# Kernel optimization log

Measured on AMD Instinct MI355X. Metric: run time of the kernel, lower is better.

Reference implementation:

```python
import jax, jax.numpy as jnp
import numpy as np

# BEV grid config from __init__ defaults
X0, XS, BX = -50.0, 0.5, 200
Y0, YS, BY = -50.0, 0.5, 200
Z0, Z1, BZ = -10.0, 10.0, 20


def setup_inputs() -> dict:
    key = jax.random.key(0)
    k1, k2, k3 = jax.random.split(key, 3)
    B, N, D, H, W, C = 2, 6, 41, 28, 50, 64
    # ego-frame 3D points; range slightly larger than BEV bounds so some are invalid
    geometry = jax.random.uniform(k1, (B, N, D, H, W, 3), minval=-60.0, maxval=60.0)
    features = jax.random.normal(k2, (B, N, C, H, W), dtype=jnp.float32)
    # depth distribution over D bins per pixel
    depth_probs = jax.nn.softmax(jax.random.normal(k3, (B, N, D, H, W)), axis=2)
    return {"geometry": geometry, "features": features, "depth_probs": depth_probs}


def _pool_one(geom, feat, depth):
    # geom: [N, D, H, W, 3], feat: [N, C, H, W], depth: [N, D, H, W]
    x, y, z = geom[..., 0], geom[..., 1], geom[..., 2]
    # torch .long() truncates toward zero -> jnp.trunc
    xi = jnp.trunc((x - X0) / XS).astype(jnp.int32)
    yi = jnp.trunc((y - Y0) / YS).astype(jnp.int32)
    zi = jnp.trunc((z - Z0) / (Z1 - Z0) * BZ).astype(jnp.int32)
    valid = (xi >= 0) & (xi < BX) & (yi >= 0) & (yi < BY) & (zi >= 0) & (zi < BZ)
    lin = jnp.where(valid, (zi * BY + yi) * BX + xi, 0).reshape(-1)   # [P]
    w = jnp.where(valid, depth, 0.0).reshape(-1)                      # [P]
    N, C, H, W = feat.shape
    D = depth.shape[1]
    # expand per-pixel features across depth bins: [N, D, H, W, C] -> [P, C]
    feat_pts = jnp.broadcast_to(
        feat.transpose(0, 2, 3, 1)[:, None], (N, D, H, W, C)
    ).reshape(-1, C)
    vals = feat_pts * w[:, None]                                      # [P, C]
    voxel = jnp.zeros((BZ * BY * BX, C), dtype=vals.dtype).at[lin].add(vals)
    voxel = voxel.reshape(BZ, BY, BX, C)
    bev = voxel.max(axis=0)                                           # [BY, BX, C]
    return bev.transpose(2, 0, 1)                                     # [C, BY, BX]


def reference(geometry, features, depth_probs):
    # -> (B, C, bev_y, bev_x)
    return jax.vmap(_pool_one)(geometry, features, depth_probs)
```

## Files before the change

### kernel.cpp

```cpp
#include <hip/hip_runtime.h>
#include <hip/hip_bf16.h>

#define CC 64
#define HW 1400
#define DHW 57400
#define NPTS 688800
#define NCOL 80000
#define KCAP 24

#define OFF_CNT    0
#define OFF_BUCKET 320000
#define OFF_FEATT  15680000

static __device__ __forceinline__ unsigned short f32_to_bf16_rne(float v) {
    unsigned int u = __float_as_uint(v);
    unsigned int r = u + 0x7fffu + ((u >> 16) & 1u);
    return (unsigned short)(r >> 16);
}
static __device__ __forceinline__ float bf16_to_f32(unsigned short h) {
    return __uint_as_float((unsigned)h << 16);
}

__global__ __launch_bounds__(256) void kz_zero(int* __restrict__ cnt) {
    int i = blockIdx.x * 256 + threadIdx.x;
    if (i < NCOL) cnt[i] = 0;
}

__global__ __launch_bounds__(256) void k01_prep(const float* __restrict__ feat,
                                                const float* __restrict__ geom,
                                                const float* __restrict__ depth,
                                                unsigned short* __restrict__ feat_t,
                                                int* __restrict__ cnt,
                                                int2* __restrict__ bucket) {
    int bid = blockIdx.x;
    if (bid < 264) {
        __shared__ float tile[64][65];
        int bn  = bid / 22;
        int hw0 = (bid % 22) * 64;
        int wv   = threadIdx.x >> 6;
        int lane = threadIdx.x & 63;
        const float* src = feat + bn * CC * HW;
        #pragma unroll
        for (int i = 0; i < 16; ++i) {
            int c = wv * 16 + i, hw = hw0 + lane;
            if (hw < HW) tile[c][lane] = src[c * HW + hw];
        }
        __syncthreads();
        unsigned short* dst = feat_t + bn * HW * CC;
        #pragma unroll
        for (int i = 0; i < 16; ++i) {
            int hwl = wv * 16 + i, hw = hw0 + hwl;
            if (hw < HW) dst[hw * CC + lane] = f32_to_bf16_rne(tile[lane][hwl]);
        }
        return;
    }

    int pt = (bid - 264) * 256 + threadIdx.x;
    if (pt >= NPTS) return;

    float x = geom[3 * pt + 0];
    float y = geom[3 * pt + 1];
    float z = geom[3 * pt + 2];
    float w = depth[pt];

    float fx = (x + 50.0f) / 0.5f;
    float fy = (y + 50.0f) / 0.5f;
    float fz = (z + 10.0f) / 20.0f * 20.0f;
    int xi = (int)fx, yi = (int)fy, zi = (int)fz;

    bool valid = (xi >= 0) & (xi < 200) & (yi >= 0) & (yi < 200) & (zi >= 0) & (zi < 20);
    if (!valid) return;

    int bn  = pt / DHW;
    int hw  = (pt - bn * DHW) % HW;
    int b   = bn / 6;
    int col = b * 40000 + yi * 200 + xi;
    int pix = bn * HW + hw;

    int idx = atomicAdd(&cnt[col], 1);
    if (idx < KCAP)
        bucket[(size_t)col * KCAP + idx] =
            make_int2(__float_as_int(w), (pix << 5) | zi);
}

__global__ __launch_bounds__(1024) void k2_pool(const int* __restrict__ cnt,
                                                const int2* __restrict__ bucket,
                                                const unsigned short* __restrict__ feat_t,
                                                float* __restrict__ out) {
    __shared__ int2  lrec[64 * KCAP];
    __shared__ int   lcnt[64];
    __shared__ float buf[64][65];
    int tid  = threadIdx.x;
    int wv   = tid >> 6;
    int lane = tid & 63;
    int b    = blockIdx.x / 625;
    int yx0  = (blockIdx.x % 625) * 64;
    int colBase = b * 40000 + yx0;

    const int2* gsrc = bucket + (size_t)colBase * KCAP;
    lrec[tid] = gsrc[tid];
    if (tid < 64 * KCAP - 1024) lrec[1024 + tid] = gsrc[1024 + tid];
    if (tid < 64) lcnt[tid] = cnt[colBase + tid];
    __syncthreads();

    int   kk[4];
    int2  r0[4];
    float f0[4];
    #pragma unroll
    for (int j = 0; j < 4; ++j) {
        int col = wv * 4 + j;
        int kj = lcnt[col];
        kj = kj > KCAP ? KCAP : kj;
        kk[j] = __builtin_amdgcn_readfirstlane(kj);
        r0[j] = lrec[col * KCAP];
        unsigned pix = kk[j] > 0 ? (((unsigned)r0[j].y) >> 5) : 0u;
        pix = __builtin_amdgcn_readfirstlane(pix);
        f0[j] = bf16_to_f32(feat_t[pix * CC + lane]);
    }

    #pragma unroll
    for (int j = 0; j < 4; ++j) {
        int col = wv * 4 + j;
        int k = kk[j];
        const int2* rec = &lrec[col * KCAP];
        float m = 0.0f;

        if (k == 1) {
            m = fmaxf(0.0f, __int_as_float(r0[j].x) * f0[j]);
        } else if (k == 2) {
            int2 r1 = rec[1];
            unsigned px1 = __builtin_amdgcn_readfirstlane(((unsigned)r1.y) >> 5);
            float f1 = bf16_to_f32(feat_t[px1 * CC + lane]);
            float p0 = __int_as_float(r0[j].x) * f0[j];
            float p1 = __int_as_float(r1.x) * f1;
            int z0 = __builtin_amdgcn_readfirstlane(r0[j].y & 31);
            int z1 = __builtin_amdgcn_readfirstlane(r1.y & 31);
            m = (z0 == z1) ? fmaxf(0.0f, p0 + p1)
                           : fmaxf(0.0f, fmaxf(p0, p1));
        } else if (k == 3) {
            int2 r1 = rec[1], r2 = rec[2];
            unsigned px1 = __builtin_amdgcn_readfirstlane(((unsigned)r1.y) >> 5);
            unsigned px2 = __builtin_amdgcn_readfirstlane(((unsigned)r2.y) >> 5);
            float f1 = bf16_to_f32(feat_t[px1 * CC + lane]);
            float f2 = bf16_to_f32(feat_t[px2 * CC + lane]);
            float p0 = __int_as_float(r0[j].x) * f0[j];
            float p1 = __int_as_float(r1.x) * f1;
            float p2 = __int_as_float(r2.x) * f2;
            int z0 = __builtin_amdgcn_readfirstlane(r0[j].y & 31);
            int z1 = __builtin_amdgcn_readfirstlane(r1.y & 31);
            int z2 = __builtin_amdgcn_readfirstlane(r2.y & 31);
            bool e01 = (z0 == z1), e02 = (z0 == z2), e12 = (z1 == z2);
            if (e01 && e12)      m = fmaxf(0.0f, p0 + p1 + p2);
            else if (e01)        m = fmaxf(fmaxf(0.0f, p0 + p1), p2);
            else if (e02)        m = fmaxf(fmaxf(0.0f, p0 + p2), p1);
            else if (e12)        m = fmaxf(fmaxf(0.0f, p0), p1 + p2);
            else                 m = fmaxf(fmaxf(0.0f, p0), fmaxf(p1, p2));
        } else if (k >= 4) {
            unsigned handled = 0;
            for (int i = 0; i < k; ++i) {
                if ((handled >> i) & 1) continue;
                int2 ri = rec[i];
                int zi = __builtin_amdgcn_readfirstlane(ri.y & 31);
                unsigned pxi = __builtin_amdgcn_readfirstlane(((unsigned)ri.y) >> 5);
                float s = __int_as_float(ri.x) * bf16_to_f32(feat_t[pxi * CC + lane]);
                for (int t = i + 1; t < k; ++t) {
                    int2 rt = rec[t];
                    if (!((handled >> t) & 1) &&
                        __builtin_amdgcn_readfirstlane(rt.y & 31) == zi) {
                        unsigned pxt = __builtin_amdgcn_readfirstlane(((unsigned)rt.y) >> 5);
                        s += __int_as_float(rt.x) * bf16_to_f32(feat_t[pxt * CC + lane]);
                        handled |= 1u << t;
                    }
                }
                m = fmaxf(m, s);
            }
        }
        buf[col][lane] = m;
    }
    __syncthreads();
    #pragma unroll
    for (int i = 0; i < 4; ++i) {
        int c = wv * 4 + i;
        out[((size_t)b * CC + c) * 40000 + yx0 + lane] = buf[lane][c];
    }
}

extern "C" void kernel_launch(void* const* d_in, const int* in_sizes, int n_in,
                              void* d_out, int out_size, void* d_ws, size_t ws_size,
                              hipStream_t stream) {
    const float* geom  = (const float*)d_in[0];
    const float* feat  = (const float*)d_in[1];
    const float* depth = (const float*)d_in[2];
    float* out = (float*)d_out;

    char* ws = (char*)d_ws;
    int*            cnt    = (int*)(ws + OFF_CNT);
    int2*           bucket = (int2*)(ws + OFF_BUCKET);
    unsigned short* feat_t = (unsigned short*)(ws + OFF_FEATT);

    hipLaunchKernelGGL(kz_zero,  dim3(313),  dim3(256),  0, stream, cnt);
    hipLaunchKernelGGL(k01_prep, dim3(2955), dim3(256),  0, stream, feat, geom, depth, feat_t, cnt, bucket);
    hipLaunchKernelGGL(k2_pool,  dim3(1250), dim3(1024), 0, stream, cnt, bucket, feat_t, out);
}
```

Before: 35.72 us.

## Split buckets into hot/overflow arrays and read records directly in pool kernel

Bucket records are split into a compact first-8 array and an overflow array. The pool kernel now reads counts and the first two records straight from global memory with one 16-byte load, instead of staging the full 24-slot bucket block in LDS. The aim is to cut the mostly wasted traffic of copying all 24 slots per column when typical counts are small. Blocks shrink to 512 threads covering 32 columns, the zeroing kernel writes int4, and the output store is remapped. The cost is extra scattered global loads for columns holding 3 or more points.

Result: slower. 37.96 us (+6.3%).

```diff
diff --git a/kernel.cpp b/kernel.cpp
--- a/kernel.cpp
+++ b/kernel.cpp
@@ -7,9 +7,11 @@
 #define NPTS 688800
 #define NCOL 80000
 #define KCAP 24
+#define KA   8
 
 #define OFF_CNT    0
-#define OFF_BUCKET 320000
+#define OFF_BUCKA  320000
+#define OFF_BUCKB  5440000
 #define OFF_FEATT  15680000
 
 static __device__ __forceinline__ unsigned short f32_to_bf16_rne(float v) {
@@ -21,9 +23,9 @@
     return __uint_as_float((unsigned)h << 16);
 }
 
-__global__ __launch_bounds__(256) void kz_zero(int* __restrict__ cnt) {
+__global__ __launch_bounds__(256) void kz_zero(int4* __restrict__ cnt4) {
     int i = blockIdx.x * 256 + threadIdx.x;
-    if (i < NCOL) cnt[i] = 0;
+    if (i < NCOL / 4) cnt4[i] = make_int4(0, 0, 0, 0);
 }
 
 __global__ __launch_bounds__(256) void k01_prep(const float* __restrict__ feat,
@@ -31,7 +33,8 @@
                                                 const float* __restrict__ depth,
                                                 unsigned short* __restrict__ feat_t,
                                                 int* __restrict__ cnt,
-                                                int2* __restrict__ bucket) {
+                                                int2* __restrict__ bucketA,
+                                                int2* __restrict__ bucketB) {
     int bid = blockIdx.x;
     if (bid < 264) {
         __shared__ float tile[64][65];
@@ -78,76 +81,69 @@
     int pix = bn * HW + hw;
 
     int idx = atomicAdd(&cnt[col], 1);
-    if (idx < KCAP)
-        bucket[(size_t)col * KCAP + idx] =
-            make_int2(__float_as_int(w), (pix << 5) | zi);
-}
-
-__global__ __launch_bounds__(1024) void k2_pool(const int* __restrict__ cnt,
-                                                const int2* __restrict__ bucket,
-                                                const unsigned short* __restrict__ feat_t,
-                                                float* __restrict__ out) {
-    __shared__ int2  lrec[64 * KCAP];
-    __shared__ int   lcnt[64];
-    __shared__ float buf[64][65];
+    int2 rec = make_int2(__float_as_int(w), (pix << 5) | zi);
+    if (idx < KA)
+        bucketA[(size_t)col * KA + idx] = rec;
+    else if (idx < KCAP)
+        bucketB[(size_t)col * (KCAP - KA) + (idx - KA)] = rec;
+}
+
+__global__ __launch_bounds__(512) void k2_pool(const int* __restrict__ cnt,
+                                               const int2* __restrict__ bucketA,
+                                               const int2* __restrict__ bucketB,
+                                               const unsigned short* __restrict__ feat_t,
+                                               float* __restrict__ out) {
+    __shared__ float buf[32][65];
     int tid  = threadIdx.x;
     int wv   = tid >> 6;
     int lane = tid & 63;
-    int b    = blockIdx.x / 625;
-    int yx0  = (blockIdx.x % 625) * 64;
+    int b    = blockIdx.x / 1250;
+    int yx0  = (blockIdx.x % 1250) * 32;
     int colBase = b * 40000 + yx0;
 
-    const int2* gsrc = bucket + (size_t)colBase * KCAP;
-    lrec[tid] = gsrc[tid];
-    if (tid < 64 * KCAP - 1024) lrec[1024 + tid] = gsrc[1024 + tid];
-    if (tid < 64) lcnt[tid] = cnt[colBase + tid];
-    __syncthreads();
-
     int   kk[4];
-    int2  r0[4];
+    int4  r01[4];
     float f0[4];
     #pragma unroll
     for (int j = 0; j < 4; ++j) {
-        int col = wv * 4 + j;
-        int kj = lcnt[col];
+        int col = colBase + wv * 4 + j;
+        int kj  = cnt[col];
         kj = kj > KCAP ? KCAP : kj;
-        kk[j] = __builtin_amdgcn_readfirstlane(kj);
-        r0[j] = lrec[col * KCAP];
-        unsigned pix = kk[j] > 0 ? (((unsigned)r0[j].y) >> 5) : 0u;
+        kk[j]  = __builtin_amdgcn_readfirstlane(kj);
+        r01[j] = *(const int4*)(bucketA + (size_t)col * KA);
+        unsigned pix = kk[j] > 0 ? (((unsigned)r01[j].y) >> 5) : 0u;
         pix = __builtin_amdgcn_readfirstlane(pix);
         f0[j] = bf16_to_f32(feat_t[pix * CC + lane]);
     }
 
     #pragma unroll
     for (int j = 0; j < 4; ++j) {
-        int col = wv * 4 + j;
+        int colLocal = wv * 4 + j;
+        int col = colBase + colLocal;
         int k = kk[j];
-        const int2* rec = &lrec[col * KCAP];
         float m = 0.0f;
 
         if (k == 1) {
-            m = fmaxf(0.0f, __int_as_float(r0[j].x) * f0[j]);
+            m = fmaxf(0.0f, __int_as_float(r01[j].x) * f0[j]);
         } else if (k == 2) {
-            int2 r1 = rec[1];
-            unsigned px1 = __builtin_amdgcn_readfirstlane(((unsigned)r1.y) >> 5);
+            unsigned px1 = __builtin_amdgcn_readfirstlane(((unsigned)r01[j].w) >> 5);
             float f1 = bf16_to_f32(feat_t[px1 * CC + lane]);
-            float p0 = __int_as_float(r0[j].x) * f0[j];
-            float p1 = __int_as_float(r1.x) * f1;
-            int z0 = __builtin_amdgcn_readfirstlane(r0[j].y & 31);
-            int z1 = __builtin_amdgcn_readfirstlane(r1.y & 31);
-            m = (z0 == z1) ? fmaxf(0.0f, p0 + p1)
-                           : fmaxf(0.0f, fmaxf(p0, p1));
+            float p0 = __int_as_float(r01[j].x) * f0[j];
+            float p1 = __int_as_float(r01[j].z) * f1;
+            int z0 = __builtin_amdgcn_readfirstlane(r01[j].y & 31);
+            int z1 = __builtin_amdgcn_readfirstlane(r01[j].w & 31);
+            m = (z0 == z1) ? fmaxf(0.0f, p0 + p1) : fmaxf(0.0f, fmaxf(p0, p1));
         } else if (k == 3) {
-            int2 r1 = rec[1], r2 = rec[2];
-            unsigned px1 = __builtin_amdgcn_readfirstlane(((unsigned)r1.y) >> 5);
+            int2 r2 = bucketA[(size_t)col * KA + 2];
+            unsigned px1 = __builtin_amdgcn_readfirstlane(((unsigned)r01[j].w) >> 5);
             unsigned px2 = __builtin_amdgcn_readfirstlane(((unsigned)r2.y) >> 5);
             float f1 = bf16_to_f32(feat_t[px1 * CC + lane]);
             float f2 = bf16_to_f32(feat_t[px2 * CC + lane]);
-            float p0 = __int_as_float(r0[j].x) * f0[j];
-            float p1 = __int_as_float(r1.x) * f1;
+            float p0 = __int_as_float(r01[j].x) * f0[j];
+            float p1 = __int_as_float(r01[j].z) * f1;
             float p2 = __int_as_float(r2.x) * f2;
-            int z0 = __builtin_amdgcn_readfirstlane(r0[j].y & 31);
-            int z1 = __builtin_amdgcn_readfirstlane(r1.y & 31);
+            int z0 = __builtin_amdgcn_readfirstlane(r01[j].y & 31);
+            int z1 = __builtin_amdgcn_readfirstlane(r01[j].w & 31);
             int z2 = __builtin_amdgcn_readfirstlane(r2.y & 31);
             bool e01 = (z0 == z1), e02 = (z0 == z2), e12 = (z1 == z2);
             if (e01 && e12)      m = fmaxf(0.0f, p0 + p1 + p2);
@@ -159,12 +155,14 @@
             unsigned handled = 0;
             for (int i = 0; i < k; ++i) {
                 if ((handled >> i) & 1) continue;
-                int2 ri = rec[i];
+                int2 ri = (i < KA) ? bucketA[(size_t)col * KA + i]
+                                   : bucketB[(size_t)col * (KCAP - KA) + (i - KA)];
                 int zi = __builtin_amdgcn_readfirstlane(ri.y & 31);
                 unsigned pxi = __builtin_amdgcn_readfirstlane(((unsigned)ri.y) >> 5);
                 float s = __int_as_float(ri.x) * bf16_to_f32(feat_t[pxi * CC + lane]);
                 for (int t = i + 1; t < k; ++t) {
-                    int2 rt = rec[t];
+                    int2 rt = (t < KA) ? bucketA[(size_t)col * KA + t]
+                                       : bucketB[(size_t)col * (KCAP - KA) + (t - KA)];
                     if (!((handled >> t) & 1) &&
                         __builtin_amdgcn_readfirstlane(rt.y & 31) == zi) {
                         unsigned pxt = __builtin_amdgcn_readfirstlane(((unsigned)rt.y) >> 5);
@@ -175,13 +173,14 @@
                 m = fmaxf(m, s);
             }
         }
-        buf[col][lane] = m;
+        buf[colLocal][lane] = m;
     }
     __syncthreads();
     #pragma unroll
     for (int i = 0; i < 4; ++i) {
-        int c = wv * 4 + i;
-        out[((size_t)b * CC + c) * 40000 + yx0 + lane] = buf[lane][c];
+        int e = i * 512 + tid;
+        int c = e >> 5, q = e & 31;
+        out[((size_t)b * CC + c) * 40000 + yx0 + q] = buf[q][c];
     }
 }
 
@@ -194,11 +193,12 @@
     float* out = (float*)d_out;
 
     char* ws = (char*)d_ws;
-    int*            cnt    = (int*)(ws + OFF_CNT);
-    int2*           bucket = (int2*)(ws + OFF_BUCKET);
-    unsigned short* feat_t = (unsigned short*)(ws + OFF_FEATT);
-
-    hipLaunchKernelGGL(kz_zero,  dim3(313),  dim3(256),  0, stream, cnt);
-    hipLaunchKernelGGL(k01_prep, dim3(2955), dim3(256),  0, stream, feat, geom, depth, feat_t, cnt, bucket);
-    hipLaunchKernelGGL(k2_pool,  dim3(1250), dim3(1024), 0, stream, cnt, bucket, feat_t, out);
-}
+    int*            cnt     = (int*)(ws + OFF_CNT);
+    int2*           bucketA = (int2*)(ws + OFF_BUCKA);
+    int2*           bucketB = (int2*)(ws + OFF_BUCKB);
+    unsigned short* feat_t  = (unsigned short*)(ws + OFF_FEATT);
+
+    hipLaunchKernelGGL(kz_zero,  dim3(79),   dim3(256), 0, stream, (int4*)cnt);
+    hipLaunchKernelGGL(k01_prep, dim3(2955), dim3(256), 0, stream, feat, geom, depth, feat_t, cnt, bucketA, bucketB);
+    hipLaunchKernelGGL(k2_pool,  dim3(2500), dim3(512), 0, stream, cnt, bucketA, bucketB, feat_t, out);
+}
```

## Split buckets into hot/overflow arrays, merge zero into transpose, vectorize binning

Applied to the files above, without the earlier changes.

Splits the per-column record store into a compact 8-slot primary array and a 16-slot overflow array, so the pool kernel stages only 8 records per column into shared memory and reads the rest from global memory only when a column holds more than 8 points. The count zeroing moves into the feature transpose kernel, which removes one launch, and point binning now loads geometry and depth as float4 with 4 points per thread. This trims pool-stage traffic and launch overhead. In exchange, the transpose now runs before binning and in a separate launch, so the two can no longer overlap as they did in the fused prep kernel.

Result: faster. 34.55 us (-3.3%).

```diff
diff --git a/kernel.cpp b/kernel.cpp
--- a/kernel.cpp
+++ b/kernel.cpp
@@ -7,9 +7,11 @@
 #define NPTS 688800
 #define NCOL 80000
 #define KCAP 24
+#define KA   8
 
 #define OFF_CNT    0
-#define OFF_BUCKET 320000
+#define OFF_BUCKA  320000
+#define OFF_BUCKB  5440000
 #define OFF_FEATT  15680000
 
 static __device__ __forceinline__ unsigned short f32_to_bf16_rne(float v) {
@@ -21,73 +23,82 @@
     return __uint_as_float((unsigned)h << 16);
 }
 
-__global__ __launch_bounds__(256) void kz_zero(int* __restrict__ cnt) {
-    int i = blockIdx.x * 256 + threadIdx.x;
-    if (i < NCOL) cnt[i] = 0;
-}
-
-__global__ __launch_bounds__(256) void k01_prep(const float* __restrict__ feat,
-                                                const float* __restrict__ geom,
-                                                const float* __restrict__ depth,
-                                                unsigned short* __restrict__ feat_t,
-                                                int* __restrict__ cnt,
-                                                int2* __restrict__ bucket) {
-    int bid = blockIdx.x;
-    if (bid < 264) {
-        __shared__ float tile[64][65];
-        int bn  = bid / 22;
-        int hw0 = (bid % 22) * 64;
-        int wv   = threadIdx.x >> 6;
-        int lane = threadIdx.x & 63;
-        const float* src = feat + bn * CC * HW;
-        #pragma unroll
-        for (int i = 0; i < 16; ++i) {
-            int c = wv * 16 + i, hw = hw0 + lane;
-            if (hw < HW) tile[c][lane] = src[c * HW + hw];
-        }
-        __syncthreads();
-        unsigned short* dst = feat_t + bn * HW * CC;
-        #pragma unroll
-        for (int i = 0; i < 16; ++i) {
-            int hwl = wv * 16 + i, hw = hw0 + hwl;
-            if (hw < HW) dst[hw * CC + lane] = f32_to_bf16_rne(tile[lane][hwl]);
-        }
-        return;
-    }
-
-    int pt = (bid - 264) * 256 + threadIdx.x;
-    if (pt >= NPTS) return;
-
-    float x = geom[3 * pt + 0];
-    float y = geom[3 * pt + 1];
-    float z = geom[3 * pt + 2];
-    float w = depth[pt];
-
-    float fx = (x + 50.0f) / 0.5f;
-    float fy = (y + 50.0f) / 0.5f;
-    float fz = (z + 10.0f) / 20.0f * 20.0f;
-    int xi = (int)fx, yi = (int)fy, zi = (int)fz;
-
-    bool valid = (xi >= 0) & (xi < 200) & (yi >= 0) & (yi < 200) & (zi >= 0) & (zi < 20);
-    if (!valid) return;
-
-    int bn  = pt / DHW;
-    int hw  = (pt - bn * DHW) % HW;
-    int b   = bn / 6;
-    int col = b * 40000 + yi * 200 + xi;
-    int pix = bn * HW + hw;
-
-    int idx = atomicAdd(&cnt[col], 1);
-    if (idx < KCAP)
-        bucket[(size_t)col * KCAP + idx] =
-            make_int2(__float_as_int(w), (pix << 5) | zi);
+__global__ __launch_bounds__(256) void k0_init_transpose(const float* __restrict__ feat,
+                                                         unsigned short* __restrict__ feat_t,
+                                                         int4* __restrict__ cnt4) {
+    for (int i = blockIdx.x * 256 + threadIdx.x; i < NCOL / 4; i += gridDim.x * 256)
+        cnt4[i] = make_int4(0, 0, 0, 0);
+
+    __shared__ float tile[64][65];
+    int bn  = blockIdx.x / 22;
+    int hw0 = (blockIdx.x % 22) * 64;
+    int wv   = threadIdx.x >> 6;
+    int lane = threadIdx.x & 63;
+    const float* src = feat + bn * CC * HW;
+    #pragma unroll
+    for (int i = 0; i < 16; ++i) {
+        int c = wv * 16 + i, hw = hw0 + lane;
+        if (hw < HW) tile[c][lane] = src[c * HW + hw];
+    }
+    __syncthreads();
+    unsigned short* dst = feat_t + bn * HW * CC;
+    #pragma unroll
+    for (int i = 0; i < 16; ++i) {
+        int hwl = wv * 16 + i, hw = hw0 + hwl;
+        if (hw < HW) dst[hw * CC + lane] = f32_to_bf16_rne(tile[lane][hwl]);
+    }
+}
+
+__global__ __launch_bounds__(256) void k1_bin(const float* __restrict__ geom,
+                                              const float* __restrict__ depth,
+                                              int* __restrict__ cnt,
+                                              int2* __restrict__ bucketA,
+                                              int2* __restrict__ bucketB) {
+    int p0 = (blockIdx.x * 256 + threadIdx.x) * 4;
+    if (p0 >= NPTS) return;
+
+    const float4* g4 = (const float4*)(geom + 3 * (size_t)p0);
+    float4 ga = g4[0], gb = g4[1], gc = g4[2];
+    float4 dw = *(const float4*)(depth + p0);
+
+    float px[4] = { ga.x, ga.w, gb.z, gc.y };
+    float py[4] = { ga.y, gb.x, gb.w, gc.z };
+    float pz[4] = { ga.z, gb.y, gc.x, gc.w };
+    float wd[4] = { dw.x, dw.y, dw.z, dw.w };
+
+    #pragma unroll
+    for (int i = 0; i < 4; ++i) {
+        float fx = (px[i] + 50.0f) / 0.5f;
+        float fy = (py[i] + 50.0f) / 0.5f;
+        float fz = (pz[i] + 10.0f) / 20.0f * 20.0f;
+        int xi = (int)fx, yi = (int)fy, zi = (int)fz;
+
+        bool valid = (xi >= 0) & (xi < 200) & (yi >= 0) & (yi < 200) &
+                     (zi >= 0) & (zi < 20);
+        if (!valid) continue;
+
+        int pt  = p0 + i;
+        int bn  = pt / DHW;
+        int hw  = (pt - bn * DHW) % HW;
+        int b   = bn / 6;
+        int col = b * 40000 + yi * 200 + xi;
+        int pix = bn * HW + hw;
+
+        int idx = atomicAdd(&cnt[col], 1);
+        int2 rec = make_int2(__float_as_int(wd[i]), (pix << 5) | zi);
+        if (idx < KA)
+            bucketA[(size_t)col * KA + idx] = rec;
+        else if (idx < KCAP)
+            bucketB[(size_t)col * (KCAP - KA) + (idx - KA)] = rec;
+    }
 }
 
 __global__ __launch_bounds__(1024) void k2_pool(const int* __restrict__ cnt,
-                                                const int2* __restrict__ bucket,
+                                                const int2* __restrict__ bucketA,
+                                                const int2* __restrict__ bucketB,
                                                 const unsigned short* __restrict__ feat_t,
                                                 float* __restrict__ out) {
-    __shared__ int2  lrec[64 * KCAP];
+    __shared__ int2  lrec[64 * KA];
     __shared__ int   lcnt[64];
     __shared__ float buf[64][65];
     int tid  = threadIdx.x;
@@ -97,9 +108,7 @@
     int yx0  = (blockIdx.x % 625) * 64;
     int colBase = b * 40000 + yx0;
 
-    const int2* gsrc = bucket + (size_t)colBase * KCAP;
-    lrec[tid] = gsrc[tid];
-    if (tid < 64 * KCAP - 1024) lrec[1024 + tid] = gsrc[1024 + tid];
+    if (tid < 64 * KA) lrec[tid] = bucketA[(size_t)colBase * KA + tid];
     if (tid < 64) lcnt[tid] = cnt[colBase + tid];
     __syncthreads();
 
@@ -112,7 +121,7 @@
         int kj = lcnt[col];
         kj = kj > KCAP ? KCAP : kj;
         kk[j] = __builtin_amdgcn_readfirstlane(kj);
-        r0[j] = lrec[col * KCAP];
+        r0[j] = lrec[col * KA];
         unsigned pix = kk[j] > 0 ? (((unsigned)r0[j].y) >> 5) : 0u;
         pix = __builtin_amdgcn_readfirstlane(pix);
         f0[j] = bf16_to_f32(feat_t[pix * CC + lane]);
@@ -120,9 +129,10 @@
 
     #pragma unroll
     for (int j = 0; j < 4; ++j) {
-        int col = wv * 4 + j;
+        int colLocal = wv * 4 + j;
+        int col = colBase + colLocal;
         int k = kk[j];
-        const int2* rec = &lrec[col * KCAP];
+        const int2* rec = &lrec[colLocal * KA];
         float m = 0.0f;
 
         if (k == 1) {
@@ -135,8 +145,7 @@
             float p1 = __int_as_float(r1.x) * f1;
             int z0 = __builtin_amdgcn_readfirstlane(r0[j].y & 31);
             int z1 = __builtin_amdgcn_readfirstlane(r1.y & 31);
-            m = (z0 == z1) ? fmaxf(0.0f, p0 + p1)
-                           : fmaxf(0.0f, fmaxf(p0, p1));
+            m = (z0 == z1) ? fmaxf(0.0f, p0 + p1) : fmaxf(0.0f, fmaxf(p0, p1));
         } else if (k == 3) {
             int2 r1 = rec[1], r2 = rec[2];
             unsigned px1 = __builtin_amdgcn_readfirstlane(((unsigned)r1.y) >> 5);
@@ -159,12 +168,14 @@
             unsigned handled = 0;
             for (int i = 0; i < k; ++i) {
                 if ((handled >> i) & 1) continue;
-                int2 ri = rec[i];
+                int2 ri = (i < KA) ? rec[i]
+                                   : bucketB[(size_t)col * (KCAP - KA) + (i - KA)];
                 int zi = __builtin_amdgcn_readfirstlane(ri.y & 31);
                 unsigned pxi = __builtin_amdgcn_readfirstlane(((unsigned)ri.y) >> 5);
                 float s = __int_as_float(ri.x) * bf16_to_f32(feat_t[pxi * CC + lane]);
                 for (int t = i + 1; t < k; ++t) {
-                    int2 rt = rec[t];
+                    int2 rt = (t < KA) ? rec[t]
+                                       : bucketB[(size_t)col * (KCAP - KA) + (t - KA)];
                     if (!((handled >> t) & 1) &&
                         __builtin_amdgcn_readfirstlane(rt.y & 31) == zi) {
                         unsigned pxt = __builtin_amdgcn_readfirstlane(((unsigned)rt.y) >> 5);
@@ -175,7 +186,7 @@
                 m = fmaxf(m, s);
             }
         }
-        buf[col][lane] = m;
+        buf[colLocal][lane] = m;
     }
     __syncthreads();
     #pragma unroll
@@ -194,11 +205,15 @@
     float* out = (float*)d_out;
 
     char* ws = (char*)d_ws;
-    int*            cnt    = (int*)(ws + OFF_CNT);
-    int2*           bucket = (int2*)(ws + OFF_BUCKET);
-    unsigned short* feat_t = (unsigned short*)(ws + OFF_FEATT);
-
-    hipLaunchKernelGGL(kz_zero,  dim3(313),  dim3(256),  0, stream, cnt);
-    hipLaunchKernelGGL(k01_prep, dim3(2955), dim3(256),  0, stream, feat, geom, depth, feat_t, cnt, bucket);
-    hipLaunchKernelGGL(k2_pool,  dim3(1250), dim3(1024), 0, stream, cnt, bucket, feat_t, out);
-}
+    int*            cnt     = (int*)(ws + OFF_CNT);
+    int2*           bucketA = (int2*)(ws + OFF_BUCKA);
+    int2*           bucketB = (int2*)(ws + OFF_BUCKB);
+    unsigned short* feat_t  = (unsigned short*)(ws + OFF_FEATT);
+
+    hipLaunchKernelGGL(k0_init_transpose, dim3(264),  dim3(256),  0, stream,
+                       feat, feat_t, (int4*)cnt);
+    hipLaunchKernelGGL(k1_bin,            dim3(673),  dim3(256),  0, stream,
+                       geom, depth, cnt, bucketA, bucketB);
+    hipLaunchKernelGGL(k2_pool,           dim3(1250), dim3(1024), 0, stream,
+                       cnt, bucketA, bucketB, feat_t, out);
+}
```
